# Kernel tuning notes

Measured on AMD Instinct MI355X. Metric: run time of the kernel, lower is better.

Reference implementation:

```python
import jax, jax.numpy as jnp
import numpy as np
import math

NUM_HEADS = 16
HEAD_DIM = 64
D_MODEL = NUM_HEADS * HEAD_DIM  # 1024
B, S = 4, 2048

def setup_inputs() -> dict:
    key = jax.random.key(0)
    ks = jax.random.split(key, 8)
    sd = 1.0 / math.sqrt(D_MODEL)
    return {
        "hidden_states": jax.random.normal(ks[0], (B, S, D_MODEL), jnp.float32),
        "attention_mask": jnp.zeros((B, 1, 1, S), jnp.float32),
        "Wq": jax.random.normal(ks[1], (D_MODEL, D_MODEL), jnp.float32) * sd,
        "bq": jnp.zeros((D_MODEL,), jnp.float32),
        "Wk": jax.random.normal(ks[2], (D_MODEL, D_MODEL), jnp.float32) * sd,
        "bk": jnp.zeros((D_MODEL,), jnp.float32),
        "Wv": jax.random.normal(ks[3], (D_MODEL, D_MODEL), jnp.float32) * sd,
        "bv": jnp.zeros((D_MODEL,), jnp.float32),
    }

def _split_heads(x):
    # [B, S, D] -> [B, H, S, hd]
    b, s, _ = x.shape
    return x.reshape(b, s, NUM_HEADS, HEAD_DIM).transpose(0, 2, 1, 3)

def reference(hidden_states, attention_mask, Wq, bq, Wk, bk, Wv, bv):
    # Linear projections (torch nn.Linear: x @ W.T + b)
    q = _split_heads(hidden_states @ Wq.T + bq)
    k = _split_heads(hidden_states @ Wk.T + bk)
    v = _split_heads(hidden_states @ Wv.T + bv)
    scale = 1.0 / math.sqrt(HEAD_DIM)
    # [B, H, Sq, Sk] attention scores, fully materialized as in the original
    scores = jnp.einsum("bhqd,bhkd->bhqk", q, k) * scale + attention_mask
    # relusq replacement for softmax
    probs = jnp.square(jax.nn.relu(scores))
    ctx = jnp.einsum("bhqk,bhkd->bhqd", probs, v)  # [B, H, S, hd]
    b = ctx.shape[0]
    return ctx.transpose(0, 2, 1, 3).reshape(b, -1, D_MODEL)
```

## Files before the change

### kernel.cpp

```cpp
#include <hip/hip_runtime.h>


typedef __bf16 bf16x8 __attribute__((ext_vector_type(8)));
typedef __bf16 bf16x4 __attribute__((ext_vector_type(4)));
typedef short  s16x4  __attribute__((ext_vector_type(4)));
typedef float  f32x4  __attribute__((ext_vector_type(4)));
typedef float  floatx4 __attribute__((ext_vector_type(4)));

#define MFMA16(a, b, c) __builtin_amdgcn_mfma_f32_16x16x32_bf16(a, b, c, 0, 0, 0)
#define MFMA16K16(a, b, c) \
    __builtin_amdgcn_mfma_f32_16x16x16bf16_1k(a, b, c, 0, 0, 0)

#define WAITCNT_VM0() __builtin_amdgcn_s_waitcnt(0x0F70)
#define BARRIER() __builtin_amdgcn_s_barrier()
#define SETPRIO(p) __builtin_amdgcn_s_setprio(p)

__device__ __forceinline__ void glds16(const __bf16* g, __bf16* l) {
    __builtin_amdgcn_global_load_lds(
        (const __attribute__((address_space(1))) void*)g,
        (__attribute__((address_space(3))) void*)l, 16, 0, 0);
}

__global__ __launch_bounds__(256) void convert_kernel(
    const float* __restrict__ X, const float* __restrict__ Wq,
    const float* __restrict__ Wk, const float* __restrict__ Wv,
    __bf16* __restrict__ Xb, __bf16* __restrict__ Wqb,
    __bf16* __restrict__ Wkb, __bf16* __restrict__ Wvb)
{
    int blk = blockIdx.x;
    const float* src; __bf16* dst; size_t base;
    if (blk < 4096)      { src = X;  dst = Xb;  base = (size_t)blk * 2048; }
    else if (blk < 4608) { src = Wq; dst = Wqb; base = (size_t)(blk - 4096) * 2048; }
    else if (blk < 5120) { src = Wk; dst = Wkb; base = (size_t)(blk - 4608) * 2048; }
    else                 { src = Wv; dst = Wvb; base = (size_t)(blk - 5120) * 2048; }
    size_t off = base + (size_t)threadIdx.x * 8;
    floatx4 a = *(const floatx4*)(src + off);
    floatx4 c = *(const floatx4*)(src + off + 4);
    bf16x8 o;
    o[0] = (__bf16)a[0]; o[1] = (__bf16)a[1]; o[2] = (__bf16)a[2]; o[3] = (__bf16)a[3];
    o[4] = (__bf16)c[0]; o[5] = (__bf16)c[1]; o[6] = (__bf16)c[2]; o[7] = (__bf16)c[3];
    *(bf16x8*)(dst + off) = o;
}

__global__ __launch_bounds__(256) void qkv_gemm_kernel(
    const __bf16* __restrict__ Xb,
    const __bf16* __restrict__ Wqb, const __bf16* __restrict__ Wkb,
    const __bf16* __restrict__ Wvb,
    const float* __restrict__ bq, const float* __restrict__ bk,
    const float* __restrict__ bv,
    __bf16* __restrict__ qws, __bf16* __restrict__ kws, __bf16* __restrict__ vws)
{
    __shared__ __bf16 As[2][128 * 64];
    __shared__ __bf16 Bs[2][128 * 64];

    const int tid  = threadIdx.x;
    const int lane = tid & 63;
    const int wave = tid >> 6;
    const int wm   = (wave >> 1) * 64;
    const int wn   = (wave & 1) * 64;
    const int quad = lane >> 4;
    const int l16  = lane & 15;
    const int m0   = blockIdx.y * 128;

    const int sel = blockIdx.x >> 3;
    const bool vmode = (sel == 2);
    const __bf16* Wb = (sel == 0) ? Wqb : (sel == 1) ? Wkb : Wvb;
    const float* bias = (sel == 0) ? bq : (sel == 1) ? bk : bv;
    __bf16* outp = (sel == 0) ? qws : (sel == 1) ? kws : vws;
    const int n0 = (blockIdx.x & 7) * 128;

    const int woffA = vmode ? wm : wn;
    const int woffB = vmode ? wn : wm;

    const int srow = lane >> 3;
    const int schk = lane & 7;

    f32x4 acc[4][4] = {};

    #pragma unroll
    for (int i = 0; i < 4; ++i) {
        int rb = wave * 32 + i * 8;
        int r  = rb + srow;
        int c  = schk ^ (r & 7);
        glds16(Xb + (size_t)(m0 + r) * 1024 + c * 8, &As[0][rb * 64]);
        glds16(Wb + (size_t)(n0 + r) * 1024 + c * 8, &Bs[0][rb * 64]);
    }
    WAITCNT_VM0();
    BARRIER();

    for (int s = 0; s < 16; ++s) {
        const int kn = ((s + 1) & 15) * 64;
        const int nb = (s + 1) & 1;
        const int bc = s & 1;
        #pragma unroll
        for (int i = 0; i < 4; ++i) {
            int rb = wave * 32 + i * 8;
            int r  = rb + srow;
            int c  = schk ^ (r & 7);
            glds16(Xb + (size_t)(m0 + r) * 1024 + kn + c * 8, &As[nb][rb * 64]);
            glds16(Wb + (size_t)(n0 + r) * 1024 + kn + c * 8, &Bs[nb][rb * 64]);
        }

        const __bf16* Pa_ = vmode ? &As[bc][0] : &Bs[bc][0];
        const __bf16* Pb_ = vmode ? &Bs[bc][0] : &As[bc][0];

        SETPRIO(1);
        #pragma unroll
        for (int kk8 = 0; kk8 < 8; kk8 += 4) {
            bf16x8 af[4], bfr[4];
            #pragma unroll
            for (int a = 0; a < 4; ++a)
                af[a] = *(const bf16x8*)&Pa_[(woffA + a * 16 + l16) * 64 +
                                             (((kk8 + quad) ^ (l16 & 7)) * 8)];
            #pragma unroll
            for (int bb = 0; bb < 4; ++bb)
                bfr[bb] = *(const bf16x8*)&Pb_[(woffB + bb * 16 + l16) * 64 +
                                               (((kk8 + quad) ^ (l16 & 7)) * 8)];
            #pragma unroll
            for (int a = 0; a < 4; ++a)
                #pragma unroll
                for (int bb = 0; bb < 4; ++bb)
                    acc[a][bb] = MFMA16(af[a], bfr[bb], acc[a][bb]);
        }
        SETPRIO(0);

        WAITCNT_VM0();
        BARRIER();
    }

    if (!vmode) {
        #pragma unroll
        for (int a = 0; a < 4; ++a) {
            int n = n0 + woffA + a * 16 + quad * 4;
            floatx4 bv4 = *(const floatx4*)&bias[n];
            int h = n >> 6, d0 = n & 63;
            #pragma unroll
            for (int bb = 0; bb < 4; ++bb) {
                int m = m0 + woffB + bb * 16 + l16;
                int bt = m >> 11, ss = m & 2047;
                bf16x4 o;
                #pragma unroll
                for (int r = 0; r < 4; ++r)
                    o[r] = (__bf16)(acc[a][bb][r] + bv4[r]);
                *(bf16x4*)&outp[((size_t)(bt * 16 + h) * 2048 + ss) * 64 + d0] = o;
            }
        }
    } else {
        #pragma unroll
        for (int a = 0; a < 4; ++a) {
            int m = m0 + woffA + a * 16 + quad * 4;
            int bt = m >> 11, s0 = m & 2047;
            #pragma unroll
            for (int bb = 0; bb < 4; ++bb) {
                int n = n0 + woffB + bb * 16 + l16;
                float bvv = bias[n];
                int h = n >> 6, d = n & 63;
                bf16x4 o;
                #pragma unroll
                for (int r = 0; r < 4; ++r)
                    o[r] = (__bf16)(acc[a][bb][r] + bvv);
                *(bf16x4*)&outp[((size_t)(bt * 16 + h) * 64 + d) * 2048 + s0] = o;
            }
        }
    }
}

__global__ __launch_bounds__(512, 4) void attn_kernel(
    const __bf16* __restrict__ Q, const __bf16* __restrict__ K,
    const __bf16* __restrict__ Vt, const float* __restrict__ mask,
    float* __restrict__ out)
{
    __shared__ __bf16 Ks[2][2][64 * 64];
    __shared__ __bf16 Vs[2][2][64 * 64];
    __shared__ float  Ms[2048];

    const int tid  = threadIdx.x;
    const int lane = tid & 63;
    const int wave = tid >> 6;
    const int quad = lane >> 4;
    const int l16  = lane & 15;
    const int bh   = blockIdx.x;
    const int b    = bh >> 4;
    const int h    = bh & 15;
    const int q0   = blockIdx.y * 256 + wave * 32;

    const __bf16* Qb = Q  + (size_t)bh * 2048 * 64;
    const __bf16* Kb = K  + (size_t)bh * 2048 * 64;
    const __bf16* Vb = Vt + (size_t)bh * 64 * 2048;
    const float*  mb = mask + b * 2048;

    const int rb = wave * 8;
    const int sr = rb + (lane >> 3);
    const int sc = ((lane & 7) ^ (sr & 7)) * 8;

    bf16x8 aq[2][2];
    #pragma unroll
    for (int qi = 0; qi < 2; ++qi)
        #pragma unroll
        for (int kcd = 0; kcd < 2; ++kcd)
            aq[qi][kcd] = *(const bf16x8*)(Qb +
                (size_t)(q0 + qi * 16 + l16) * 64 + kcd * 32 + quad * 8);

    f32x4 co[2][4] = {};

    glds16(Kb + (size_t)sr * 64 + sc,        &Ks[0][0][rb * 64]);
    glds16(Kb + (size_t)(64 + sr) * 64 + sc, &Ks[0][1][rb * 64]);
    glds16(Vb + (size_t)sr * 2048 + sc,      &Vs[0][0][rb * 64]);
    glds16(Vb + (size_t)sr * 2048 + 64 + sc, &Vs[0][1][rb * 64]);
    glds16((const __bf16*)mb + (size_t)wave * 512 + lane * 8,
           (__bf16*)Ms + wave * 512);
    WAITCNT_VM0();
    BARRIER();

    for (int t = 0; t < 16; ++t) {
        const int kn = ((t + 1) & 15) * 128;
        const int nb = (t + 1) & 1;
        const int cb = t & 1;
        glds16(Kb + (size_t)(kn + sr) * 64 + sc,       &Ks[nb][0][rb * 64]);
        glds16(Kb + (size_t)(kn + 64 + sr) * 64 + sc,  &Ks[nb][1][rb * 64]);
        glds16(Vb + (size_t)sr * 2048 + kn + sc,       &Vs[nb][0][rb * 64]);
        glds16(Vb + (size_t)sr * 2048 + kn + 64 + sc,  &Vs[nb][1][rb * 64]);

        #pragma unroll
        for (int hf = 0; hf < 2; ++hf) {
            const __bf16* Kt = &Ks[cb][hf][0];
            const __bf16* Vtile = &Vs[cb][hf][0];
            const int k0 = t * 128 + hf * 64;

            f32x4 st[4][2] = {};
            SETPRIO(1);
            #pragma unroll
            for (int ki = 0; ki < 4; ++ki) {
                #pragma unroll
                for (int kcd = 0; kcd < 2; ++kcd) {
                    int key = ki * 16 + l16;
                    bf16x8 ak = *(const bf16x8*)&Kt[key * 64 +
                        (((kcd * 4 + quad) ^ (key & 7)) * 8)];
                    #pragma unroll
                    for (int qi = 0; qi < 2; ++qi)
                        st[ki][qi] = MFMA16(ak, aq[qi][kcd], st[ki][qi]);
                }
            }
            SETPRIO(0);

            bf16x4 pf[4][2];
            const f32x4 zero4 = {};
            #pragma unroll
            for (int ki = 0; ki < 4; ++ki) {
                f32x4 mk = *(const f32x4*)&Ms[k0 + ki * 16 + quad * 4];
                #pragma unroll
                for (int qi = 0; qi < 2; ++qi) {
                    f32x4 x = st[ki][qi] * 0.125f + mk;
                    x = __builtin_elementwise_max(x, zero4);
                    x = x * x;
                    bf16x4 pv;
                    pv[0] = (__bf16)x[0]; pv[1] = (__bf16)x[1];
                    pv[2] = (__bf16)x[2]; pv[3] = (__bf16)x[3];
                    pf[ki][qi] = pv;
                }
            }

            SETPRIO(1);
            #pragma unroll
            for (int ki = 0; ki < 4; ++ki) {
                bf16x4 vb4[4];
                #pragma unroll
                for (int dt = 0; dt < 4; ++dt) {
                    int d = dt * 16 + l16;
                    int g = ki * 2 + (quad >> 1);
                    vb4[dt] = *(const bf16x4*)&Vtile[d * 64 +
                        ((g ^ (d & 7)) * 8) + (quad & 1) * 4];
                }
                #pragma unroll
                for (int qi = 0; qi < 2; ++qi) {
                    s16x4 pa = __builtin_bit_cast(s16x4, pf[ki][qi]);
                    #pragma unroll
                    for (int dt = 0; dt < 4; ++dt)
                        co[qi][dt] = MFMA16K16(pa,
                            __builtin_bit_cast(s16x4, vb4[dt]), co[qi][dt]);
                }
            }
            SETPRIO(0);
        }

        WAITCNT_VM0();
        BARRIER();
    }

    #pragma unroll
    for (int qi = 0; qi < 2; ++qi)
        #pragma unroll
        for (int r = 0; r < 4; ++r) {
            int q = q0 + qi * 16 + quad * 4 + r;
            float* orow = &out[(((size_t)b * 2048 + q) * 16 + h) * 64];
            #pragma unroll
            for (int dt = 0; dt < 4; ++dt)
                orow[dt * 16 + l16] = co[qi][dt][r];
        }
}

extern "C" void kernel_launch(void* const* d_in, const int* in_sizes, int n_in,
                              void* d_out, int out_size, void* d_ws, size_t ws_size,
                              hipStream_t stream) {
    const float* hidden = (const float*)d_in[0];
    const float* mask   = (const float*)d_in[1];
    const float* Wq     = (const float*)d_in[2];
    const float* bq     = (const float*)d_in[3];
    const float* Wk     = (const float*)d_in[4];
    const float* bk     = (const float*)d_in[5];
    const float* Wv     = (const float*)d_in[6];
    const float* bv     = (const float*)d_in[7];
    float* out = (float*)d_out;

    __bf16* qws = (__bf16*)d_ws;
    __bf16* kws = qws + (size_t)64 * 2048 * 64;
    __bf16* vws = kws + (size_t)64 * 2048 * 64;
    __bf16* Xb  = vws + (size_t)64 * 2048 * 64;
    __bf16* Wqb = Xb  + (size_t)8192 * 1024;
    __bf16* Wkb = Wqb + (size_t)1024 * 1024;
    __bf16* Wvb = Wkb + (size_t)1024 * 1024;

    convert_kernel<<<dim3(5632), dim3(256), 0, stream>>>(hidden, Wq, Wk, Wv,
                                                         Xb, Wqb, Wkb, Wvb);
    qkv_gemm_kernel<<<dim3(24, 64), dim3(256), 0, stream>>>(Xb, Wqb, Wkb, Wvb,
                                                            bq, bk, bv,
                                                            qws, kws, vws);
    attn_kernel<<<dim3(64, 8), dim3(512), 0, stream>>>(qws, kws, vws, mask, out);
}
```

Before: 250.4 us.

## Switch attention MFMAs to 32x32x16 bf16 tiles with permlane32 swap relayout

Recasts the QK^T and PV products in the attention kernel from 16x16 MFMAs (including the older 16x16x16 variant for PV) to 32x32x16 bf16 MFMAs. The probability fragments are rearranged between lane halves with permlane32_swap so the score accumulator layout can feed the second MFMA directly. LDS reads are widened to 8-element loads, and the output store is remapped to the 32x32 accumulator layout. The goal is fewer MFMA instructions and LDS reads per tile, at the cost of larger accumulators and more register pressure.

Measured after the change: 241.3 us. 1.04x faster.

```diff
diff --git a/kernel.cpp b/kernel.cpp
--- a/kernel.cpp
+++ b/kernel.cpp
@@ -3,13 +3,16 @@
 
 typedef __bf16 bf16x8 __attribute__((ext_vector_type(8)));
 typedef __bf16 bf16x4 __attribute__((ext_vector_type(4)));
+typedef __bf16 bf16x2 __attribute__((ext_vector_type(2)));
 typedef short  s16x4  __attribute__((ext_vector_type(4)));
 typedef float  f32x4  __attribute__((ext_vector_type(4)));
+typedef float  f32x16 __attribute__((ext_vector_type(16)));
 typedef float  floatx4 __attribute__((ext_vector_type(4)));
+typedef unsigned u32x2 __attribute__((ext_vector_type(2)));
+typedef unsigned u32x4 __attribute__((ext_vector_type(4)));
 
 #define MFMA16(a, b, c) __builtin_amdgcn_mfma_f32_16x16x32_bf16(a, b, c, 0, 0, 0)
-#define MFMA16K16(a, b, c) \
-    __builtin_amdgcn_mfma_f32_16x16x16bf16_1k(a, b, c, 0, 0, 0)
+#define MFMA32(a, b, c) __builtin_amdgcn_mfma_f32_32x32x16_bf16(a, b, c, 0, 0, 0)
 
 #define WAITCNT_VM0() __builtin_amdgcn_s_waitcnt(0x0F70)
 #define BARRIER() __builtin_amdgcn_s_barrier()
@@ -177,12 +180,12 @@
     const int tid  = threadIdx.x;
     const int lane = tid & 63;
     const int wave = tid >> 6;
-    const int quad = lane >> 4;
-    const int l16  = lane & 15;
+    const int l32  = lane & 31;
+    const int hi   = lane >> 5;
     const int bh   = blockIdx.x;
     const int b    = bh >> 4;
     const int h    = bh & 15;
-    const int q0   = blockIdx.y * 256 + wave * 32;
+    const int q0w  = blockIdx.y * 256 + wave * 32;
 
     const __bf16* Qb = Q  + (size_t)bh * 2048 * 64;
     const __bf16* Kb = K  + (size_t)bh * 2048 * 64;
@@ -193,15 +196,13 @@
     const int sr = rb + (lane >> 3);
     const int sc = ((lane & 7) ^ (sr & 7)) * 8;
 
-    bf16x8 aq[2][2];
+    bf16x8 aq[4];
     #pragma unroll
-    for (int qi = 0; qi < 2; ++qi)
-        #pragma unroll
-        for (int kcd = 0; kcd < 2; ++kcd)
-            aq[qi][kcd] = *(const bf16x8*)(Qb +
-                (size_t)(q0 + qi * 16 + l16) * 64 + kcd * 32 + quad * 8);
-
-    f32x4 co[2][4] = {};
+    for (int dk = 0; dk < 4; ++dk)
+        aq[dk] = *(const bf16x8*)(Qb +
+            (size_t)(q0w + l32) * 64 + dk * 16 + hi * 8);
+
+    f32x16 co0 = {}, co1 = {};
 
     glds16(Kb + (size_t)sr * 64 + sc,        &Ks[0][0][rb * 64]);
     glds16(Kb + (size_t)(64 + sr) * 64 + sc, &Ks[0][1][rb * 64]);
@@ -224,63 +225,70 @@
         #pragma unroll
         for (int hf = 0; hf < 2; ++hf) {
             const __bf16* Kt = &Ks[cb][hf][0];
-            const __bf16* Vtile = &Vs[cb][hf][0];
+            const __bf16* Vtl = &Vs[cb][hf][0];
             const int k0 = t * 128 + hf * 64;
 
-            f32x4 st[4][2] = {};
+            f32x16 st0 = {}, st1 = {};
             SETPRIO(1);
             #pragma unroll
-            for (int ki = 0; ki < 4; ++ki) {
-                #pragma unroll
-                for (int kcd = 0; kcd < 2; ++kcd) {
-                    int key = ki * 16 + l16;
-                    bf16x8 ak = *(const bf16x8*)&Kt[key * 64 +
-                        (((kcd * 4 + quad) ^ (key & 7)) * 8)];
-                    #pragma unroll
-                    for (int qi = 0; qi < 2; ++qi)
-                        st[ki][qi] = MFMA16(ak, aq[qi][kcd], st[ki][qi]);
-                }
+            for (int dk = 0; dk < 4; ++dk) {
+                const int g = dk * 2 + hi;
+                const int c0 = (g ^ (l32 & 7)) * 8;
+                bf16x8 ak0 = *(const bf16x8*)&Kt[l32 * 64 + c0];
+                bf16x8 ak1 = *(const bf16x8*)&Kt[(32 + l32) * 64 + c0];
+                st0 = MFMA32(ak0, aq[dk], st0);
+                st1 = MFMA32(ak1, aq[dk], st1);
             }
             SETPRIO(0);
 
-            bf16x4 pf[4][2];
-            const f32x4 zero4 = {};
-            #pragma unroll
-            for (int ki = 0; ki < 4; ++ki) {
-                f32x4 mk = *(const f32x4*)&Ms[k0 + ki * 16 + quad * 4];
-                #pragma unroll
-                for (int qi = 0; qi < 2; ++qi) {
-                    f32x4 x = st[ki][qi] * 0.125f + mk;
-                    x = __builtin_elementwise_max(x, zero4);
-                    x = x * x;
-                    bf16x4 pv;
-                    pv[0] = (__bf16)x[0]; pv[1] = (__bf16)x[1];
-                    pv[2] = (__bf16)x[2]; pv[3] = (__bf16)x[3];
-                    pf[ki][qi] = pv;
+            #pragma unroll
+            for (int kg = 0; kg < 2; ++kg) {
+                const f32x16 s = kg ? st1 : st0;
+                const f32x4 zero4 = {};
+                unsigned W[4][2];
+                #pragma unroll
+                for (int G = 0; G < 4; ++G) {
+                    f32x4 v;
+                    v[0] = s[G * 4 + 0]; v[1] = s[G * 4 + 1];
+                    v[2] = s[G * 4 + 2]; v[3] = s[G * 4 + 3];
+                    f32x4 mk = *(const f32x4*)&Ms[k0 + kg * 32 + G * 8 + hi * 4];
+                    v = v * 0.125f + mk;
+                    v = __builtin_elementwise_max(v, zero4);
+                    v = v * v;
+                    bf16x2 w0, w1;
+                    w0[0] = (__bf16)v[0]; w0[1] = (__bf16)v[1];
+                    w1[0] = (__bf16)v[2]; w1[1] = (__bf16)v[3];
+                    W[G][0] = __builtin_bit_cast(unsigned, w0);
+                    W[G][1] = __builtin_bit_cast(unsigned, w1);
                 }
+                u32x2 s00 = __builtin_amdgcn_permlane32_swap(W[0][0], W[1][0], false, false);
+                u32x2 s01 = __builtin_amdgcn_permlane32_swap(W[0][1], W[1][1], false, false);
+                u32x2 s10 = __builtin_amdgcn_permlane32_swap(W[2][0], W[3][0], false, false);
+                u32x2 s11 = __builtin_amdgcn_permlane32_swap(W[2][1], W[3][1], false, false);
+                u32x4 f0, f1;
+                f0[0] = s00[0]; f0[1] = s01[0]; f0[2] = s00[1]; f0[3] = s01[1];
+                f1[0] = s10[0]; f1[1] = s11[0]; f1[2] = s10[1]; f1[3] = s11[1];
+                bf16x8 pa0 = __builtin_bit_cast(bf16x8, f0);
+                bf16x8 pa1 = __builtin_bit_cast(bf16x8, f1);
+
+                SETPRIO(1);
+                #pragma unroll
+                for (int dt = 0; dt < 2; ++dt) {
+                    const int d = dt * 32 + l32;
+                    const int ch0 = (kg * 4 + hi) ^ (d & 7);
+                    const int ch1 = (kg * 4 + 2 + hi) ^ (d & 7);
+                    bf16x8 vb0 = *(const bf16x8*)&Vtl[d * 64 + ch0 * 8];
+                    bf16x8 vb1 = *(const bf16x8*)&Vtl[d * 64 + ch1 * 8];
+                    if (dt == 0) {
+                        co0 = MFMA32(pa0, vb0, co0);
+                        co0 = MFMA32(pa1, vb1, co0);
+                    } else {
+                        co1 = MFMA32(pa0, vb0, co1);
+                        co1 = MFMA32(pa1, vb1, co1);
+                    }
+                }
+                SETPRIO(0);
             }
-
-            SETPRIO(1);
-            #pragma unroll
-            for (int ki = 0; ki < 4; ++ki) {
-                bf16x4 vb4[4];
-                #pragma unroll
-                for (int dt = 0; dt < 4; ++dt) {
-                    int d = dt * 16 + l16;
-                    int g = ki * 2 + (quad >> 1);
-                    vb4[dt] = *(const bf16x4*)&Vtile[d * 64 +
-                        ((g ^ (d & 7)) * 8) + (quad & 1) * 4];
-                }
-                #pragma unroll
-                for (int qi = 0; qi < 2; ++qi) {
-                    s16x4 pa = __builtin_bit_cast(s16x4, pf[ki][qi]);
-                    #pragma unroll
-                    for (int dt = 0; dt < 4; ++dt)
-                        co[qi][dt] = MFMA16K16(pa,
-                            __builtin_bit_cast(s16x4, vb4[dt]), co[qi][dt]);
-                }
-            }
-            SETPRIO(0);
         }
 
         WAITCNT_VM0();
@@ -288,15 +296,12 @@
     }
 
     #pragma unroll
-    for (int qi = 0; qi < 2; ++qi)
-        #pragma unroll
-        for (int r = 0; r < 4; ++r) {
-            int q = q0 + qi * 16 + quad * 4 + r;
-            float* orow = &out[(((size_t)b * 2048 + q) * 16 + h) * 64];
-            #pragma unroll
-            for (int dt = 0; dt < 4; ++dt)
-                orow[dt * 16 + l16] = co[qi][dt][r];
-        }
+    for (int r = 0; r < 16; ++r) {
+        int q = q0w + (r & 3) + 8 * (r >> 2) + 4 * hi;
+        float* orow = &out[(((size_t)b * 2048 + q) * 16 + h) * 64];
+        orow[l32]      = co0[r];
+        orow[32 + l32] = co1[r];
+    }
 }
 
 extern "C" void kernel_launch(void* const* d_in, const int* in_sizes, int n_in,
```
